# Kernel optimization log

Hardware: AMD Instinct MI355X
Metric: run time of the kernel (lower is better)

## Reference

```python
import jax, jax.numpy as jnp
import numpy as np

EPS = 1e-5

def _layernorm(x, g, b):
    mu = jnp.mean(x, axis=-1, keepdims=True)
    var = jnp.mean((x - mu) ** 2, axis=-1, keepdims=True)
    return (x - mu) * jax.lax.rsqrt(var + EPS) * g + b

def setup_inputs() -> dict:
    key = jax.random.key(0)
    ks = jax.random.split(key, 12)
    B, N, C, n = 2, 1024, 256, 100
    x = jax.random.normal(ks[0], (B, N, C), dtype=jnp.float32)
    query = jax.random.normal(ks[1], (n, B, C), dtype=jnp.float32)
    policy = jax.random.uniform(ks[2], (B, N, 1), dtype=jnp.float32)
    s = lambda k, shp: jax.random.normal(k, shp, dtype=jnp.float32) * (1.0 / np.sqrt(shp[0]))
    return {
        "x": x, "query": query, "policy": policy,
        "ln_g": jnp.ones((C,), jnp.float32), "ln_b": jnp.zeros((C,), jnp.float32),
        "W_in": s(ks[3], (C, C)), "b_in": jnp.zeros((C,), jnp.float32),
        "W1": s(ks[4], (2 * C, C)), "b1": jnp.zeros((C,), jnp.float32),
        "W2": s(ks[5], (C, C // 2)), "b2": jnp.zeros((C // 2,), jnp.float32),
        "W3": s(ks[6], (C // 2, 2)), "b3": jnp.zeros((2,), jnp.float32),
    }

def reference(x, query, policy, ln_g, ln_b, W_in, b_in, W1, b1, W2, b2, W3, b3):
    B, N, C = x.shape
    n = query.shape[0]
    q = jnp.transpose(query, (1, 0, 2))  # [B, n, C]
    # in_conv: LayerNorm -> Linear -> GELU. The torch code repeats x across the
    # query dim first, but the math is identical per query, so compute once.
    h = jax.nn.gelu(_layernorm(x, ln_g, ln_b) @ W_in + b_in, approximate=False)  # [B, N, C]
    half = C // 2
    local_x = h[:, :, :half]  # [B, N, C/2]
    # policy-weighted masked pooling (policy identical across queries)
    glob = jnp.sum(h[:, :, half:] * policy, axis=1, keepdims=True) / jnp.sum(policy, axis=1, keepdims=True)  # [B, 1, C/2]
    feature = jnp.concatenate([
        jnp.broadcast_to(local_x[:, None, :, :], (B, n, N, half)),
        jnp.broadcast_to(glob[:, None, :, :], (B, n, N, half)),
        jnp.broadcast_to(q[:, :, None, :], (B, n, N, C)),
    ], axis=-1)  # [B, n, N, 2C]
    z = jax.nn.gelu(feature @ W1 + b1, approximate=False)
    z = jax.nn.gelu(z @ W2 + b2, approximate=False)
    z = z @ W3 + b3
    return jax.nn.log_softmax(z, axis=-1)  # [B, n, N, 2]
```

## Files before the change

### kernel.cpp

```cpp
#include <hip/hip_runtime.h>
#include <math.h>

#define BB 2
#define NN 1024
#define CC 256
#define NQ 100
#define HALF 128

typedef __attribute__((ext_vector_type(8))) short bf16x8;
typedef __attribute__((ext_vector_type(4))) float f32x4;

__device__ __forceinline__ float gelu_fast(float x) {
    float a = fabsf(0.70710678118654752f * x);
    float t = fmaf(a, 4.30638e-5f, 2.765672e-4f);
    t = fmaf(a, t, 1.520143e-4f);
    t = fmaf(a, t, 9.2705272e-3f);
    t = fmaf(a, t, 4.22820123e-2f);
    t = fmaf(a, t, 7.05230784e-2f);
    float p = fmaf(a, t, 1.0f);
    float p2 = p * p;
    float p4 = p2 * p2;
    float p8 = p4 * p4;
    float p16 = p8 * p8;
    float r = 0.5f * __builtin_amdgcn_rcpf(p16);
    float phi = (x >= 0.0f) ? (1.0f - r) : r;
    return x * phi;
}

__device__ __forceinline__ short f2bf(float f) {
    union { float f; unsigned u; } v; v.f = f;
    return (short)((v.u + 0x7FFFu + ((v.u >> 16) & 1u)) >> 16);
}

__global__ __launch_bounds__(256) void kA_fused(
        const float* __restrict__ x, const float* __restrict__ ln_g,
        const float* __restrict__ ln_b, const float* __restrict__ W_in,
        const float* __restrict__ b_in, const float* __restrict__ policy,
        const float* __restrict__ W1, float* __restrict__ At,
        float* __restrict__ gsum, float* __restrict__ psum) {
    __shared__ float xst[CC][4];
    __shared__ float hst[HALF][4];
    int t = threadIdx.x;
    int wave = t >> 6, lane = t & 63;
    int row0 = blockIdx.x * 4;
    const float* xr = x + (size_t)(row0 + wave) * CC;
    float v0 = xr[lane], v1 = xr[lane + 64], v2 = xr[lane + 128], v3 = xr[lane + 192];
    float s = v0 + v1 + v2 + v3;
    for (int off = 32; off; off >>= 1) s += __shfl_down(s, off);
    s = __shfl(s, 0);
    float mu = s * (1.0f / CC);
    float d0 = v0 - mu, d1 = v1 - mu, d2 = v2 - mu, d3 = v3 - mu;
    float vs = d0 * d0 + d1 * d1 + d2 * d2 + d3 * d3;
    for (int off = 32; off; off >>= 1) vs += __shfl_down(vs, off);
    vs = __shfl(vs, 0);
    float rstd = rsqrtf(vs * (1.0f / CC) + 1e-5f);
    xst[lane][wave]       = d0 * rstd * ln_g[lane]       + ln_b[lane];
    xst[lane + 64][wave]  = d1 * rstd * ln_g[lane + 64]  + ln_b[lane + 64];
    xst[lane + 128][wave] = d2 * rstd * ln_g[lane + 128] + ln_b[lane + 128];
    xst[lane + 192][wave] = d3 * rstd * ln_g[lane + 192] + ln_b[lane + 192];
    __syncthreads();
    float a0 = b_in[t], a1 = a0, a2 = a0, a3 = a0;
    #pragma unroll 8
    for (int k = 0; k < CC; ++k) {
        float4 xv = *(const float4*)xst[k];
        float wv = W_in[k * CC + t];
        a0 = fmaf(xv.x, wv, a0); a1 = fmaf(xv.y, wv, a1);
        a2 = fmaf(xv.z, wv, a2); a3 = fmaf(xv.w, wv, a3);
    }
    float h0 = gelu_fast(a0), h1 = gelu_fast(a1), h2 = gelu_fast(a2), h3 = gelu_fast(a3);
    float p0 = policy[row0], p1 = policy[row0 + 1], p2 = policy[row0 + 2], p3 = policy[row0 + 3];
    int b = row0 >> 10;
    if (t < HALF) {
        hst[t][0] = h0; hst[t][1] = h1; hst[t][2] = h2; hst[t][3] = h3;
    } else {
        atomicAdd(&gsum[b * HALF + (t - HALF)], h0 * p0 + h1 * p1 + h2 * p2 + h3 * p3);
    }
    if (t == 0) atomicAdd(&psum[b], p0 + p1 + p2 + p3);
    __syncthreads();
    float c0 = 0, c1 = 0, c2 = 0, c3 = 0;
    #pragma unroll 8
    for (int k = 0; k < HALF; ++k) {
        float4 hv = *(const float4*)hst[k];
        float wv = W1[k * CC + t];
        c0 = fmaf(hv.x, wv, c0); c1 = fmaf(hv.y, wv, c1);
        c2 = fmaf(hv.z, wv, c2); c3 = fmaf(hv.w, wv, c3);
    }
    int lr = row0 & (NN - 1);
    size_t tb = ((size_t)(b * 64 + (lr >> 4)) * 32 + (t >> 3)) * 128 + (t & 7);
    int r16 = lr & 15;
    At[tb + (r16 + 0) * 8] = c0;
    At[tb + (r16 + 1) * 8] = c1;
    At[tb + (r16 + 2) * 8] = c2;
    At[tb + (r16 + 3) * 8] = c3;
}

__global__ __launch_bounds__(256) void kB_qc_prep(
        const float* __restrict__ query, const float* __restrict__ W1,
        const float* __restrict__ W2, const float* __restrict__ gsum,
        const float* __restrict__ psum, const float* __restrict__ b1,
        float* __restrict__ Qc, short* __restrict__ W2T) {
    int blk = blockIdx.x, t = threadIdx.x;
    if (blk < BB * NQ) {
        __shared__ float gl[HALF];
        __shared__ float qs[CC];
        int b = blk / NQ, i = blk % NQ;
        if (t < HALF) gl[t] = gsum[b * HALF + t] / psum[b];
        qs[t] = query[(size_t)(i * BB + b) * CC + t];
        __syncthreads();
        float g = b1[t];
        #pragma unroll 8
        for (int k = 0; k < HALF; ++k) g = fmaf(gl[k], W1[(HALF + k) * CC + t], g);
        #pragma unroll 8
        for (int k = 0; k < CC; ++k) g = fmaf(qs[k], W1[(2 * HALF + k) * CC + t], g);
        Qc[(size_t)blk * CC + t] = g;
    } else {
        int u = (blk - BB * NQ) * 256 + t;
        int c = u >> 6, kg = u & 63;
        short4 v;
        v.x = f2bf(W2[(kg * 4 + 0) * HALF + c]);
        v.y = f2bf(W2[(kg * 4 + 1) * HALF + c]);
        v.z = f2bf(W2[(kg * 4 + 2) * HALF + c]);
        v.w = f2bf(W2[(kg * 4 + 3) * HALF + c]);
        *(short4*)(W2T + c * CC + kg * 4) = v;
    }
}

#define W2S 72

__global__ __launch_bounds__(256, 4) void k5_main(
        const float* __restrict__ At, const float* __restrict__ Qc,
        const short* __restrict__ W2T, const float* __restrict__ b2,
        const float* __restrict__ W3, const float* __restrict__ b3,
        float* __restrict__ out) {
    __shared__ short w2s[128 * W2S];

    int t = threadIdx.x;
    int lane = t & 63, w = t >> 6;
    int col16 = lane & 15, quad = lane >> 4;
    int blk = blockIdx.x;
    int jt = blk & 15;
    int iq = (blk >> 4) % NQ;
    int b  = blk / (16 * NQ);
    const float* Abase = At + ((size_t)(b * 64 + jt * 4 + w) * 32) * 128 + col16 * 8;
    const float* Qrow = Qc + (size_t)(b * NQ + iq) * CC;

    f32x4 acc[8];
    #pragma unroll
    for (int ni = 0; ni < 8; ++ni) acc[ni] = (f32x4){0.f, 0.f, 0.f, 0.f};

    for (int kt = 0; kt < 4; ++kt) {
        __syncthreads();
        #pragma unroll
        for (int e = 0; e < 4; ++e) {
            int u = e * 256 + t;
            int n = u >> 3, kg = u & 7;
            *(bf16x8*)&w2s[n * W2S + kg * 8] =
                *(const bf16x8*)(W2T + n * CC + kt * 64 + kg * 8);
        }
        __syncthreads();
        #pragma unroll
        for (int ks = 0; ks < 2; ++ks) {
            int k0 = kt * 64 + ks * 32 + quad * 8;
            float4 q0 = *(const float4*)(Qrow + k0);
            float4 q1 = *(const float4*)(Qrow + k0 + 4);
            const float* Ap = Abase + (size_t)(kt * 8 + ks * 4 + quad) * 128;
            float4 a0 = *(const float4*)(Ap);
            float4 a1 = *(const float4*)(Ap + 4);
            union { bf16x8 v; short s[8]; } u;
            u.s[0] = f2bf(gelu_fast(a0.x + q0.x));
            u.s[1] = f2bf(gelu_fast(a0.y + q0.y));
            u.s[2] = f2bf(gelu_fast(a0.z + q0.z));
            u.s[3] = f2bf(gelu_fast(a0.w + q0.w));
            u.s[4] = f2bf(gelu_fast(a1.x + q1.x));
            u.s[5] = f2bf(gelu_fast(a1.y + q1.y));
            u.s[6] = f2bf(gelu_fast(a1.z + q1.z));
            u.s[7] = f2bf(gelu_fast(a1.w + q1.w));
            int klocal = ks * 32 + quad * 8;
            #pragma unroll
            for (int ni = 0; ni < 8; ++ni) {
                bf16x8 bfv = *(const bf16x8*)&w2s[(ni * 16 + col16) * W2S + klocal];
                acc[ni] = __builtin_amdgcn_mfma_f32_16x16x32_bf16(u.v, bfv, acc[ni], 0, 0, 0);
            }
        }
    }

    float p0[4] = {0, 0, 0, 0}, p1[4] = {0, 0, 0, 0};
    #pragma unroll
    for (int ni = 0; ni < 8; ++ni) {
        int c = ni * 16 + col16;
        float bb = b2[c];
        float2 w3v = *(const float2*)(W3 + c * 2);
        #pragma unroll
        for (int r = 0; r < 4; ++r) {
            float z = gelu_fast(acc[ni][r] + bb);
            p0[r] = fmaf(z, w3v.x, p0[r]);
            p1[r] = fmaf(z, w3v.y, p1[r]);
        }
    }
    float b30 = b3[0], b31 = b3[1];
    #pragma unroll
    for (int r = 0; r < 4; ++r) {
        float s0 = p0[r], s1 = p1[r];
        #pragma unroll
        for (int off = 1; off < 16; off <<= 1) {
            s0 += __shfl_xor(s0, off);
            s1 += __shfl_xor(s1, off);
        }
        if (col16 == 0) {
            float z0 = s0 + b30, z1v = s1 + b31;
            float m = fmaxf(z0, z1v);
            float lse = m + __logf(__expf(z0 - m) + __expf(z1v - m));
            int j = jt * 64 + w * 16 + quad * 4 + r;
            *(float2*)(out + ((size_t)(b * NQ + iq) * NN + j) * 2) =
                make_float2(z0 - lse, z1v - lse);
        }
    }
}

extern "C" void kernel_launch(void* const* d_in, const int* in_sizes, int n_in,
                              void* d_out, int out_size, void* d_ws, size_t ws_size,
                              hipStream_t stream) {
    const float* x      = (const float*)d_in[0];
    const float* query  = (const float*)d_in[1];
    const float* policy = (const float*)d_in[2];
    const float* ln_g   = (const float*)d_in[3];
    const float* ln_b   = (const float*)d_in[4];
    const float* W_in   = (const float*)d_in[5];
    const float* b_in   = (const float*)d_in[6];
    const float* W1     = (const float*)d_in[7];
    const float* b1     = (const float*)d_in[8];
    const float* W2     = (const float*)d_in[9];
    const float* b2     = (const float*)d_in[10];
    const float* W3     = (const float*)d_in[11];
    const float* b3     = (const float*)d_in[12];
    float* out = (float*)d_out;

    float* ws    = (float*)d_ws;
    float* At    = ws;
    float* Qc    = ws + 524288;
    float* gsum  = ws + 575488;
    float* psum  = ws + 575744;
    short* W2T   = (short*)(ws + 575746 + 62);

    hipMemsetAsync(gsum, 0, (2 * HALF + 2) * sizeof(float), stream);
    kA_fused<<<(BB * NN) / 4, 256, 0, stream>>>(x, ln_g, ln_b, W_in, b_in, policy,
                                                W1, At, gsum, psum);
    kB_qc_prep<<<BB * NQ + 32, 256, 0, stream>>>(query, W1, W2, gsum, psum, b1, Qc, W2T);
    k5_main<<<BB * NQ * (NN / 64), 256, 0, stream>>>(At, Qc, W2T, b2, W3, b3, out);
}
```

Before: 173.9 us.

## Double-buffer W2 tiles in main kernel and replace atomics with partial sums

The main MFMA kernel now stages W2 in 32-wide k tiles with two shared-memory buffers. It prefetches the next tile into registers while computing the current one, so each step needs one barrier instead of two, and the smaller tile raises the occupancy hint from 4 to 6. The pooling atomics and the memset are replaced by per-block partial sums that the Qc kernel reduces. The W2 bf16 transpose moves into the first kernel's extra blocks. This trades the atomic contention and the memset launch for more global partial traffic and a serial 256-step reduction in kB.

```diff
diff --git a/kernel.cpp b/kernel.cpp
--- a/kernel.cpp
+++ b/kernel.cpp
@@ -36,13 +36,26 @@
         const float* __restrict__ x, const float* __restrict__ ln_g,
         const float* __restrict__ ln_b, const float* __restrict__ W_in,
         const float* __restrict__ b_in, const float* __restrict__ policy,
-        const float* __restrict__ W1, float* __restrict__ At,
-        float* __restrict__ gsum, float* __restrict__ psum) {
+        const float* __restrict__ W1, const float* __restrict__ W2,
+        float* __restrict__ At, float* __restrict__ gpart,
+        float* __restrict__ ppart, short* __restrict__ W2T) {
+    int t = threadIdx.x;
+    int blk = blockIdx.x;
+    if (blk >= 512) {
+        int u = (blk - 512) * 256 + t;
+        int c = u >> 6, kg = u & 63;
+        short4 v;
+        v.x = f2bf(W2[(kg * 4 + 0) * HALF + c]);
+        v.y = f2bf(W2[(kg * 4 + 1) * HALF + c]);
+        v.z = f2bf(W2[(kg * 4 + 2) * HALF + c]);
+        v.w = f2bf(W2[(kg * 4 + 3) * HALF + c]);
+        *(short4*)(W2T + c * CC + kg * 4) = v;
+        return;
+    }
     __shared__ float xst[CC][4];
     __shared__ float hst[HALF][4];
-    int t = threadIdx.x;
     int wave = t >> 6, lane = t & 63;
-    int row0 = blockIdx.x * 4;
+    int row0 = blk * 4;
     const float* xr = x + (size_t)(row0 + wave) * CC;
     float v0 = xr[lane], v1 = xr[lane + 64], v2 = xr[lane + 128], v3 = xr[lane + 192];
     float s = v0 + v1 + v2 + v3;
@@ -69,13 +82,12 @@
     }
     float h0 = gelu_fast(a0), h1 = gelu_fast(a1), h2 = gelu_fast(a2), h3 = gelu_fast(a3);
     float p0 = policy[row0], p1 = policy[row0 + 1], p2 = policy[row0 + 2], p3 = policy[row0 + 3];
-    int b = row0 >> 10;
     if (t < HALF) {
         hst[t][0] = h0; hst[t][1] = h1; hst[t][2] = h2; hst[t][3] = h3;
     } else {
-        atomicAdd(&gsum[b * HALF + (t - HALF)], h0 * p0 + h1 * p1 + h2 * p2 + h3 * p3);
-    }
-    if (t == 0) atomicAdd(&psum[b], p0 + p1 + p2 + p3);
+        gpart[(size_t)blk * HALF + (t - HALF)] = h0 * p0 + h1 * p1 + h2 * p2 + h3 * p3;
+    }
+    if (t == 0) ppart[blk] = p0 + p1 + p2 + p3;
     __syncthreads();
     float c0 = 0, c1 = 0, c2 = 0, c3 = 0;
     #pragma unroll 8
@@ -85,6 +97,7 @@
         c0 = fmaf(hv.x, wv, c0); c1 = fmaf(hv.y, wv, c1);
         c2 = fmaf(hv.z, wv, c2); c3 = fmaf(hv.w, wv, c3);
     }
+    int b = row0 >> 10;
     int lr = row0 & (NN - 1);
     size_t tb = ((size_t)(b * 64 + (lr >> 4)) * 32 + (t >> 3)) * 128 + (t & 7);
     int r16 = lr & 15;
@@ -94,45 +107,49 @@
     At[tb + (r16 + 3) * 8] = c3;
 }
 
-__global__ __launch_bounds__(256) void kB_qc_prep(
+__global__ __launch_bounds__(256) void kB_qc(
         const float* __restrict__ query, const float* __restrict__ W1,
-        const float* __restrict__ W2, const float* __restrict__ gsum,
-        const float* __restrict__ psum, const float* __restrict__ b1,
-        float* __restrict__ Qc, short* __restrict__ W2T) {
+        const float* __restrict__ gpart, const float* __restrict__ ppart,
+        const float* __restrict__ b1, float* __restrict__ Qc) {
+    __shared__ float gls[HALF];
+    __shared__ float qs[CC];
+    __shared__ float psS;
     int blk = blockIdx.x, t = threadIdx.x;
-    if (blk < BB * NQ) {
-        __shared__ float gl[HALF];
-        __shared__ float qs[CC];
-        int b = blk / NQ, i = blk % NQ;
-        if (t < HALF) gl[t] = gsum[b * HALF + t] / psum[b];
-        qs[t] = query[(size_t)(i * BB + b) * CC + t];
-        __syncthreads();
-        float g = b1[t];
+    int b = blk / NQ, i = blk % NQ;
+    if (t < 64) {
+        const float* pp = ppart + b * 256;
+        float ps = pp[t] + pp[t + 64] + pp[t + 128] + pp[t + 192];
+        for (int off = 32; off; off >>= 1) ps += __shfl_down(ps, off);
+        if (t == 0) psS = ps;
+    }
+    if (t < HALF) {
+        const float* gp = gpart + (size_t)b * 256 * HALF + t;
+        float s = 0.f;
         #pragma unroll 8
-        for (int k = 0; k < HALF; ++k) g = fmaf(gl[k], W1[(HALF + k) * CC + t], g);
-        #pragma unroll 8
-        for (int k = 0; k < CC; ++k) g = fmaf(qs[k], W1[(2 * HALF + k) * CC + t], g);
-        Qc[(size_t)blk * CC + t] = g;
-    } else {
-        int u = (blk - BB * NQ) * 256 + t;
-        int c = u >> 6, kg = u & 63;
-        short4 v;
-        v.x = f2bf(W2[(kg * 4 + 0) * HALF + c]);
-        v.y = f2bf(W2[(kg * 4 + 1) * HALF + c]);
-        v.z = f2bf(W2[(kg * 4 + 2) * HALF + c]);
-        v.w = f2bf(W2[(kg * 4 + 3) * HALF + c]);
-        *(short4*)(W2T + c * CC + kg * 4) = v;
-    }
-}
-
-#define W2S 72
-
-__global__ __launch_bounds__(256, 4) void k5_main(
+        for (int ch = 0; ch < 256; ++ch) s += gp[ch * HALF];
+        gls[t] = s;
+    }
+    qs[t] = query[(size_t)(i * BB + b) * CC + t];
+    __syncthreads();
+    float inv_ps = 1.0f / psS;
+    float g = b1[t];
+    #pragma unroll 8
+    for (int k = 0; k < HALF; ++k)
+        g = fmaf(gls[k] * inv_ps, W1[(HALF + k) * CC + t], g);
+    #pragma unroll 8
+    for (int k = 0; k < CC; ++k)
+        g = fmaf(qs[k], W1[(2 * HALF + k) * CC + t], g);
+    Qc[(size_t)blk * CC + t] = g;
+}
+
+#define W2S 40
+
+__global__ __launch_bounds__(256, 6) void k5_main(
         const float* __restrict__ At, const float* __restrict__ Qc,
         const short* __restrict__ W2T, const float* __restrict__ b2,
         const float* __restrict__ W3, const float* __restrict__ b3,
         float* __restrict__ out) {
-    __shared__ short w2s[128 * W2S];
+    __shared__ short w2s[2][128 * W2S];
 
     int t = threadIdx.x;
     int lane = t & 63, w = t >> 6;
@@ -144,43 +161,58 @@
     const float* Abase = At + ((size_t)(b * 64 + jt * 4 + w) * 32) * 128 + col16 * 8;
     const float* Qrow = Qc + (size_t)(b * NQ + iq) * CC;
 
+    int sn = t >> 2, skg = t & 3;
+    const short* Wg0 = W2T + sn * CC + skg * 8;
+    const short* Wg1 = W2T + (64 + sn) * CC + skg * 8;
+    short* Ws0 = (short*)w2s + sn * W2S + skg * 8;
+    short* Ws1 = (short*)w2s + (64 + sn) * W2S + skg * 8;
+
     f32x4 acc[8];
     #pragma unroll
     for (int ni = 0; ni < 8; ++ni) acc[ni] = (f32x4){0.f, 0.f, 0.f, 0.f};
 
-    for (int kt = 0; kt < 4; ++kt) {
-        __syncthreads();
+    {
+        bf16x8 r0 = *(const bf16x8*)(Wg0);
+        bf16x8 r1 = *(const bf16x8*)(Wg1);
+        *(bf16x8*)(Ws0) = r0;
+        *(bf16x8*)(Ws1) = r1;
+    }
+    __syncthreads();
+
+    #pragma unroll
+    for (int kt = 0; kt < 8; ++kt) {
+        int buf = kt & 1;
+        bf16x8 nx0, nx1;
+        if (kt < 7) {
+            nx0 = *(const bf16x8*)(Wg0 + (kt + 1) * 32);
+            nx1 = *(const bf16x8*)(Wg1 + (kt + 1) * 32);
+        }
+        int k0 = kt * 32 + quad * 8;
+        float4 q0 = *(const float4*)(Qrow + k0);
+        float4 q1 = *(const float4*)(Qrow + k0 + 4);
+        const float* Ap = Abase + (size_t)(kt * 4 + quad) * 128;
+        float4 a0 = *(const float4*)(Ap);
+        float4 a1 = *(const float4*)(Ap + 4);
+        union { bf16x8 v; short s[8]; } u;
+        u.s[0] = f2bf(gelu_fast(a0.x + q0.x));
+        u.s[1] = f2bf(gelu_fast(a0.y + q0.y));
+        u.s[2] = f2bf(gelu_fast(a0.z + q0.z));
+        u.s[3] = f2bf(gelu_fast(a0.w + q0.w));
+        u.s[4] = f2bf(gelu_fast(a1.x + q1.x));
+        u.s[5] = f2bf(gelu_fast(a1.y + q1.y));
+        u.s[6] = f2bf(gelu_fast(a1.z + q1.z));
+        u.s[7] = f2bf(gelu_fast(a1.w + q1.w));
         #pragma unroll
-        for (int e = 0; e < 4; ++e) {
-            int u = e * 256 + t;
-            int n = u >> 3, kg = u & 7;
-            *(bf16x8*)&w2s[n * W2S + kg * 8] =
-                *(const bf16x8*)(W2T + n * CC + kt * 64 + kg * 8);
-        }
-        __syncthreads();
-        #pragma unroll
-        for (int ks = 0; ks < 2; ++ks) {
-            int k0 = kt * 64 + ks * 32 + quad * 8;
-            float4 q0 = *(const float4*)(Qrow + k0);
-            float4 q1 = *(const float4*)(Qrow + k0 + 4);
-            const float* Ap = Abase + (size_t)(kt * 8 + ks * 4 + quad) * 128;
-            float4 a0 = *(const float4*)(Ap);
-            float4 a1 = *(const float4*)(Ap + 4);
-            union { bf16x8 v; short s[8]; } u;
-            u.s[0] = f2bf(gelu_fast(a0.x + q0.x));
-            u.s[1] = f2bf(gelu_fast(a0.y + q0.y));
-            u.s[2] = f2bf(gelu_fast(a0.z + q0.z));
-            u.s[3] = f2bf(gelu_fast(a0.w + q0.w));
-            u.s[4] = f2bf(gelu_fast(a1.x + q1.x));
-            u.s[5] = f2bf(gelu_fast(a1.y + q1.y));
-            u.s[6] = f2bf(gelu_fast(a1.z + q1.z));
-            u.s[7] = f2bf(gelu_fast(a1.w + q1.w));
-            int klocal = ks * 32 + quad * 8;
-            #pragma unroll
-            for (int ni = 0; ni < 8; ++ni) {
-                bf16x8 bfv = *(const bf16x8*)&w2s[(ni * 16 + col16) * W2S + klocal];
-                acc[ni] = __builtin_amdgcn_mfma_f32_16x16x32_bf16(u.v, bfv, acc[ni], 0, 0, 0);
-            }
+        for (int ni = 0; ni < 8; ++ni) {
+            bf16x8 bfv = *(const bf16x8*)&w2s[buf][(ni * 16 + col16) * W2S + quad * 8];
+            acc[ni] = __builtin_amdgcn_mfma_f32_16x16x32_bf16(u.v, bfv, acc[ni], 0, 0, 0);
+        }
+        if (kt < 7) {
+            short* d0 = Ws0 + (1 - buf) * 128 * W2S;
+            short* d1 = Ws1 + (1 - buf) * 128 * W2S;
+            *(bf16x8*)d0 = nx0;
+            *(bf16x8*)d1 = nx1;
+            __syncthreads();
         }
     }
 
@@ -238,13 +270,12 @@
     float* ws    = (float*)d_ws;
     float* At    = ws;
     float* Qc    = ws + 524288;
-    float* gsum  = ws + 575488;
-    float* psum  = ws + 575744;
-    short* W2T   = (short*)(ws + 575746 + 62);
-
-    hipMemsetAsync(gsum, 0, (2 * HALF + 2) * sizeof(float), stream);
-    kA_fused<<<(BB * NN) / 4, 256, 0, stream>>>(x, ln_g, ln_b, W_in, b_in, policy,
-                                                W1, At, gsum, psum);
-    kB_qc_prep<<<BB * NQ + 32, 256, 0, stream>>>(query, W1, W2, gsum, psum, b1, Qc, W2T);
+    float* gpart = ws + 575488;
+    float* ppart = ws + 641024;
+    short* W2T   = (short*)(ws + 641536);
+
+    kA_fused<<<544, 256, 0, stream>>>(x, ln_g, ln_b, W_in, b_in, policy,
+                                      W1, W2, At, gpart, ppart, W2T);
+    kB_qc<<<BB * NQ, 256, 0, stream>>>(query, W1, gpart, ppart, b1, Qc);
     k5_main<<<BB * NQ * (NN / 64), 256, 0, stream>>>(At, Qc, W2T, b2, W3, b3, out);
 }
```

New measurement: 174.6 us. No clear change (+0.4%).
